# Kernel tuning notes

Measured on AMD Instinct MI355X. Metric: run time of the kernel, lower is better.

## Reference

```python
import jax, jax.numpy as jnp
import numpy as np

B, N, D, H, SEEDS = 32, 2048, 256, 8, 32
DH = D // H
SCALE = 1.0 / np.sqrt(D)  # 1/sqrt(dim_V), as in MAB


def setup_inputs() -> dict:
    key = jax.random.key(0)
    ks = jax.random.split(key, 7)
    w_std = 1.0 / np.sqrt(D)  # ~ xavier scale for (D, D)
    x = jax.random.normal(ks[0], (B, N, D), dtype=jnp.float32)
    lengths = jax.random.randint(ks[1], (B,), 1, N + 1).astype(jnp.int64)
    S = jax.random.normal(ks[2], (1, SEEDS, D), dtype=jnp.float32) * w_std
    Wq = jax.random.normal(ks[3], (D, D), dtype=jnp.float32) * w_std
    Wk = jax.random.normal(ks[4], (D, D), dtype=jnp.float32) * w_std
    Wv = jax.random.normal(ks[5], (D, D), dtype=jnp.float32) * w_std
    Wo = jax.random.normal(ks[6], (D, D), dtype=jnp.float32) * w_std
    return {"x": x, "lengths": lengths, "S": S, "Wq": Wq, "Wk": Wk, "Wv": Wv, "Wo": Wo}


def reference(x, lengths, S, Wq, Wk, Wv, Wo):
    # PMA with norm=None: seeds attend over the (length-masked) input set.
    b, n, d = x.shape
    seeds = S.shape[1]
    # Linear projections (torch Linear: y = x @ W.T, bias=False)
    Q = jnp.einsum("bsd,ed->bse", jnp.broadcast_to(S, (b, seeds, d)), Wq)  # (B,SEEDS,D)
    K = jnp.einsum("bnd,ed->bne", x, Wk)  # (B,N,D)
    V = jnp.einsum("bnd,ed->bne", x, Wv)
    # mask=['K'] -> zero K,V rows beyond lengths
    col_mask = (jnp.arange(n)[None, :] < lengths[:, None]).astype(x.dtype)  # (B,N)
    K = K * col_mask[:, :, None]
    V = V * col_mask[:, :, None]
    # head split: (h b) s d  <=>  b h s d
    Qh = Q.reshape(b, seeds, H, DH).transpose(0, 2, 1, 3)  # (B,H,SEEDS,DH)
    Kh = K.reshape(b, n, H, DH).transpose(0, 2, 1, 3)      # (B,H,N,DH)
    Vh = V.reshape(b, n, H, DH).transpose(0, 2, 1, 3)
    scores = jnp.einsum("bhsd,bhnd->bhsn", Qh, Kh) * SCALE  # (B,H,SEEDS,N)
    exp = jnp.exp(scores)
    # set_softmax: two-sided length masks, normalize over keys with +1e-15
    row_mask = (jnp.arange(seeds)[None, :] < lengths[:, None]).astype(x.dtype)  # (B,SEEDS)
    exp = exp * row_mask[:, None, :, None] * col_mask[:, None, None, :]
    A = exp / (exp.sum(axis=3, keepdims=True) + 1e-15)
    Oh = Qh + jnp.einsum("bhsn,bhnd->bhsd", A, Vh)  # residual on Q_
    O = Oh.transpose(0, 2, 1, 3).reshape(b, seeds, d)  # merge heads
    # norm0/norm1 are None (norm=None in PMA)
    O = O + jax.nn.relu(jnp.einsum("bse,de->bsd", O, Wo))
    O = O * row_mask[:, :, None]  # final apply_masks(O, lengths)
    lengths_out = jnp.minimum(jnp.full_like(lengths, seeds), lengths)
    return O, lengths_out
```

## Files before the change

### kernel.cpp

```cpp
#include <hip/hip_runtime.h>
#include <hip/hip_bf16.h>
#include <cstdint>

#define BATCH 32
#define NKEY 2048
#define DIM 256
#define NHEAD 8
#define SEEDS 32
#define DHEAD 32
#define SCALE 0.0625f
#define NCHUNK 16
#define KCH 128
#define KT 32
#define PART_BYTES 17408

typedef unsigned short u16;
typedef __attribute__((ext_vector_type(8))) short s16x8;
typedef __attribute__((ext_vector_type(8))) unsigned short u16x8;
typedef __attribute__((ext_vector_type(4))) unsigned short u16x4;
typedef __attribute__((ext_vector_type(4))) float f32x4;

__device__ __forceinline__ u16 f2bf(float f) {
    unsigned u = __float_as_uint(f);
    u += 0x7FFFu + ((u >> 16) & 1u);
    return (u16)(u >> 16);
}
__device__ __forceinline__ float bf2f(u16 h) {
    return __uint_as_float(((unsigned)h) << 16);
}
__device__ __forceinline__ int get_len(const int* lens, int b) {
    return (lens[1] == 0) ? lens[2 * b] : lens[b];
}
__device__ __forceinline__ u16x8 cvt8(const float* p) {
    f32x4 a = *(const f32x4*)p;
    f32x4 b = *(const f32x4*)(p + 4);
    u16x8 r;
    r[0] = f2bf(a[0]); r[1] = f2bf(a[1]); r[2] = f2bf(a[2]); r[3] = f2bf(a[3]);
    r[4] = f2bf(b[0]); r[5] = f2bf(b[1]); r[6] = f2bf(b[2]); r[7] = f2bf(b[3]);
    return r;
}
__device__ __forceinline__ void glds16(const u16* g, u16* l) {
    __builtin_amdgcn_global_load_lds(
        (const __attribute__((address_space(1))) unsigned int*)g,
        (__attribute__((address_space(3))) unsigned int*)l, 16, 0, 0);
}

#define XGROUPS 2097152
#define WGROUPS 16384
#define CVTBLK 2048
__global__ __launch_bounds__(256) void cvt_kernel(const float* __restrict__ x,
                                                  const float* __restrict__ Wk,
                                                  const float* __restrict__ Wv,
                                                  const float* __restrict__ S,
                                                  const float* __restrict__ Wq,
                                                  u16* __restrict__ xb,
                                                  u16* __restrict__ wb,
                                                  float* __restrict__ qf) {
    if (blockIdx.x >= CVTBLK) {
        int s = blockIdx.x - CVTBLK;
        int e = threadIdx.x;
        __shared__ float srow[DIM];
        srow[e] = S[s * DIM + e];
        __syncthreads();
        const float* wr = Wq + (size_t)e * DIM;
        float acc = 0.f;
#pragma unroll 4
        for (int d = 0; d < DIM; d += 4) {
            f32x4 w = *(const f32x4*)(wr + d);
            acc += srow[d] * w[0] + srow[d + 1] * w[1] + srow[d + 2] * w[2] + srow[d + 3] * w[3];
        }
        qf[s * DIM + e] = acc;
        return;
    }
    size_t g = (size_t)blockIdx.x * 256 + threadIdx.x;
    const size_t stride = (size_t)CVTBLK * 256;
    for (; g < XGROUPS + WGROUPS; g += stride) {
        const float* src;
        u16* dst;
        if (g < XGROUPS) {
            src = x + g * 8;
            dst = xb + g * 8;
        } else {
            size_t gw = g - XGROUPS;
            dst = wb + gw * 8;
            src = (gw < 8192) ? (Wk + gw * 8) : (Wv + (gw - 8192) * 8);
        }
        *(u16x8*)dst = cvt8(src);
    }
}

#define BM 128
#define BN 128
#define BK 32

__global__ __launch_bounds__(256) void kv_gemm_kernel(const u16* __restrict__ xb,
                                                      const u16* __restrict__ wb,
                                                      u16* __restrict__ kg,
                                                      u16* __restrict__ vt) {
    __shared__ u16 Alds[2][BM * BK];
    __shared__ u16 Blds[2][BM * BK];
    int bid = blockIdx.x;
    int swz = (bid & 7) * 256 + (bid >> 3);
    int nb = swz & 3;
    int mb = swz >> 2;
    const u16* asrc = xb + (size_t)mb * BM * DIM;
    const u16* bsrc = wb + (size_t)nb * BN * DIM;

    int tid = threadIdx.x;
    int lane = tid & 63;
    int wid = tid >> 6;
    int wr = wid >> 1, wc = wid & 1;
    int k8 = (lane >> 4) * 8;
    int fr = lane & 15;

    int srow = wid * 32 + (lane >> 2);
    int scol = (lane & 3) * 8;
    const u16* ga0 = asrc + (size_t)srow * DIM + scol;
    const u16* gb0 = bsrc + (size_t)srow * DIM + scol;

    f32x4 acc[4][4];
#pragma unroll
    for (int m = 0; m < 4; m++)
#pragma unroll
        for (int n = 0; n < 4; n++) acc[m][n] = (f32x4){0.f, 0.f, 0.f, 0.f};

    glds16(ga0,            &Alds[0][(wid * 32) * BK]);
    glds16(ga0 + 16 * DIM, &Alds[0][(wid * 32 + 16) * BK]);
    glds16(gb0,            &Blds[0][(wid * 32) * BK]);
    glds16(gb0 + 16 * DIM, &Blds[0][(wid * 32 + 16) * BK]);
    __syncthreads();

    for (int t = 0; t < DIM / BK; t++) {
        int cur = t & 1;
        if (t + 1 < DIM / BK) {
            const u16* ga = ga0 + (t + 1) * BK;
            const u16* gb = gb0 + (t + 1) * BK;
            glds16(ga,            &Alds[cur ^ 1][(wid * 32) * BK]);
            glds16(ga + 16 * DIM, &Alds[cur ^ 1][(wid * 32 + 16) * BK]);
            glds16(gb,            &Blds[cur ^ 1][(wid * 32) * BK]);
            glds16(gb + 16 * DIM, &Blds[cur ^ 1][(wid * 32 + 16) * BK]);
        }
        s16x8 af[4], bfg[4];
#pragma unroll
        for (int m = 0; m < 4; m++)
            af[m] = *(const s16x8*)&Alds[cur][(wr * 64 + m * 16 + fr) * BK + k8];
#pragma unroll
        for (int n = 0; n < 4; n++)
            bfg[n] = *(const s16x8*)&Blds[cur][(wc * 64 + n * 16 + fr) * BK + k8];
#pragma unroll
        for (int m = 0; m < 4; m++)
#pragma unroll
            for (int n = 0; n < 4; n++)
                acc[m][n] = __builtin_amdgcn_mfma_f32_16x16x32_bf16(af[m], bfg[n], acc[m][n], 0, 0, 0);
        __syncthreads();
    }

    int gmbase = mb * BM + wr * 64 + (lane >> 4) * 4;
    int gnbase = nb * BN + wc * 64 + fr;
#pragma unroll
    for (int m = 0; m < 4; m++) {
        int r0 = gmbase + m * 16;
#pragma unroll
        for (int n = 0; n < 4; n++) {
            int gc = gnbase + n * 16;
            if (gc < 256) {
#pragma unroll
                for (int q = 0; q < 4; q++) {
                    int r = r0 + q;
                    kg[(size_t)r * 256 + (gc ^ ((r & 7) << 3))] = f2bf(acc[m][n][q]);
                }
            } else {
                int dh = gc - 256;
                int bidx = r0 >> 11, key = r0 & 2047;
                u16x4 v = {f2bf(acc[m][n][0]), f2bf(acc[m][n][1]),
                           f2bf(acc[m][n][2]), f2bf(acc[m][n][3])};
                *(u16x4*)&vt[((size_t)bidx * 256 + dh) * NKEY + key] = v;
            }
        }
    }
}

__global__ __launch_bounds__(512) void attn_kernel(const u16* __restrict__ kg,
                                                   const u16* __restrict__ vt,
                                                   const float* __restrict__ qf,
                                                   const int* __restrict__ lens,
                                                   char* __restrict__ partials) {
    int b = blockIdx.y, chunk = blockIdx.x;
    int len = get_len(lens, b);
    int n0 = chunk * KCH;
    int n1 = min(n0 + KCH, len);
    int tid = threadIdx.x;
    int lane = tid & 63;
    int h = tid >> 6;
    int fr = lane & 15;
    int g = lane >> 4;
    int k8 = g * 8;

    __shared__ u16 Klds[2][KT * 256];
    __shared__ u16 VTlds[2][256 * KT];
    __shared__ u16 Plds[NHEAD][32][32];

    s16x8 qb[2];
    qb[0] = (s16x8)cvt8(qf + (size_t)(fr) * DIM + h * DHEAD + k8);
    qb[1] = (s16x8)cvt8(qf + (size_t)(16 + fr) * DIM + h * DHEAD + k8);

    f32x4 accp[2][2];
#pragma unroll
    for (int i = 0; i < 2; i++)
#pragma unroll
        for (int j = 0; j < 2; j++) accp[i][j] = (f32x4){0.f, 0.f, 0.f, 0.f};
    float dsum[2] = {0.f, 0.f};

    int nk = n1 - n0;
    int nsteps = (nk > 0) ? ((nk + KT - 1) / KT) : 0;

    const u16* gk0 = kg + ((size_t)(b * NKEY + n0 + h * 4) + (lane >> 5)) * 256 + (lane & 31) * 8;
    const u16* gv0 = vt + ((size_t)b * 256 + h * 32 + (lane >> 2)) * NKEY + n0 + (lane & 3) * 8;

    if (nsteps > 0) {
        glds16(gk0,             &Klds[0][(h * 4) * 256]);
        glds16(gk0 + 2 * 256,   &Klds[0][(h * 4 + 2) * 256]);
        glds16(gv0,             &VTlds[0][(h * 32) * KT]);
        glds16(gv0 + 16 * NKEY, &VTlds[0][(h * 32 + 16) * KT]);
        __syncthreads();
    }

    for (int t = 0; t < nsteps; t++) {
        int cur = t & 1;
        if (t + 1 < nsteps) {
            const u16* gk = gk0 + (size_t)(t + 1) * KT * 256;
            const u16* gv = gv0 + (t + 1) * KT;
            glds16(gk,             &Klds[cur ^ 1][(h * 4) * 256]);
            glds16(gk + 2 * 256,   &Klds[cur ^ 1][(h * 4 + 2) * 256]);
            glds16(gv,             &VTlds[cur ^ 1][(h * 32) * KT]);
            glds16(gv + 16 * NKEY, &VTlds[cur ^ 1][(h * 32 + 16) * KT]);
        }

        int rem = nk - t * KT;

        s16x8 ka[2];
#pragma unroll
        for (int m = 0; m < 2; m++)
            ka[m] = *(const s16x8*)&Klds[cur][(m * 16 + fr) * 256 + (((h * 4 + g) ^ (fr & 7)) << 3)];
        f32x4 sc[2][2];
#pragma unroll
        for (int m = 0; m < 2; m++)
#pragma unroll
            for (int n = 0; n < 2; n++) {
                f32x4 z = (f32x4){0.f, 0.f, 0.f, 0.f};
                sc[m][n] = __builtin_amdgcn_mfma_f32_16x16x32_bf16(ka[m], qb[n], z, 0, 0, 0);
            }

#pragma unroll
        for (int m = 0; m < 2; m++) {
            int kbase = m * 16 + g * 4;
            int col = (((kbase >> 3) ^ (fr & 3)) << 3) + (kbase & 7);
#pragma unroll
            for (int n = 0; n < 2; n++) {
                u16x4 pv;
#pragma unroll
                for (int q = 0; q < 4; q++) {
                    float e = (kbase + q < rem) ? __expf(sc[m][n][q] * SCALE) : 0.f;
                    dsum[n] += e;
                    pv[q] = f2bf(e);
                }
                *(u16x4*)&Plds[h][n * 16 + fr][col] = pv;
            }
        }

        s16x8 pa[2], vb[2];
        int rcol = (g ^ (fr & 3)) << 3;
#pragma unroll
        for (int m = 0; m < 2; m++)
            pa[m] = *(const s16x8*)&Plds[h][m * 16 + fr][rcol];
#pragma unroll
        for (int n = 0; n < 2; n++)
            vb[n] = *(const s16x8*)&VTlds[cur][(h * 32 + n * 16 + fr) * KT + k8];
#pragma unroll
        for (int m = 0; m < 2; m++)
#pragma unroll
            for (int n = 0; n < 2; n++)
                accp[m][n] = __builtin_amdgcn_mfma_f32_16x16x32_bf16(pa[m], vb[n], accp[m][n], 0, 0, 0);
        __syncthreads();
    }

    dsum[0] += __shfl_xor(dsum[0], 16);
    dsum[0] += __shfl_xor(dsum[0], 32);
    dsum[1] += __shfl_xor(dsum[1], 16);
    dsum[1] += __shfl_xor(dsum[1], 32);

    char* pb = partials + ((size_t)b * NCHUNK + chunk) * PART_BYTES;
    u16* pnum = (u16*)pb;
    float* pden = (float*)(pb + 16384);
#pragma unroll
    for (int m = 0; m < 2; m++)
#pragma unroll
        for (int n = 0; n < 2; n++)
#pragma unroll
            for (int q = 0; q < 4; q++)
                pnum[(size_t)(m * 16 + g * 4 + q) * DIM + h * DHEAD + n * 16 + fr] =
                    f2bf(accp[m][n][q]);
    if (lane < 16) {
        pden[h * 32 + fr] = dsum[0];
        pden[h * 32 + 16 + fr] = dsum[1];
    }
}

__global__ __launch_bounds__(256) void reduce_kernel(const char* __restrict__ partials,
                                                     const float* __restrict__ qf,
                                                     const int* __restrict__ lens,
                                                     float* __restrict__ opre,
                                                     float* __restrict__ outlen) {
    int b = blockIdx.x;
    int p = threadIdx.x;
    int h = p >> 5, s = p & 31;
    float denom = 0.f;
    float num[DHEAD];
#pragma unroll
    for (int j = 0; j < DHEAD; j++) num[j] = 0.f;
    for (int c = 0; c < NCHUNK; c++) {
        const char* pb = partials + ((size_t)b * NCHUNK + c) * PART_BYTES;
        denom += ((const float*)(pb + 16384))[p];
        const u16* pn = (const u16*)pb;
#pragma unroll
        for (int j = 0; j < DHEAD; j += 8) {
            u16x8 u = *(const u16x8*)&pn[(size_t)s * DIM + h * DHEAD + j];
#pragma unroll
            for (int t = 0; t < 8; t++) num[j + t] += bf2f(u[t]);
        }
    }
    float inv = 1.f / (denom + 1e-15f);
    size_t obase = ((size_t)b * SEEDS + s) * DIM + h * DHEAD;
#pragma unroll
    for (int j = 0; j < DHEAD; j++) {
        opre[obase + j] = qf[s * DIM + h * DHEAD + j] + num[j] * inv;
    }
    if (p == 0) outlen[b] = (float)min(SEEDS, get_len(lens, b));
}

__global__ __launch_bounds__(256) void epilogue_kernel(const float* __restrict__ opre,
                                                       const float* __restrict__ Wo,
                                                       const int* __restrict__ lens,
                                                       float* __restrict__ out) {
    int s = blockIdx.x, b = blockIdx.y;
    int d = threadIdx.x;
    size_t rbase = ((size_t)b * SEEDS + s) * DIM;
    if (s >= get_len(lens, b)) {
        out[rbase + d] = 0.f;
        return;
    }
    __shared__ float orow[DIM];
    orow[d] = opre[rbase + d];
    __syncthreads();
    const float* wrow = Wo + (size_t)d * DIM;
    float acc = 0.f;
#pragma unroll 4
    for (int e = 0; e < DIM; e += 4) {
        f32x4 w = *(const f32x4*)(wrow + e);
        acc += orow[e] * w[0] + orow[e + 1] * w[1] + orow[e + 2] * w[2] + orow[e + 3] * w[3];
    }
    out[rbase + d] = orow[d] + fmaxf(acc, 0.f);
}

extern "C" void kernel_launch(void* const* d_in, const int* in_sizes, int n_in,
                              void* d_out, int out_size, void* d_ws, size_t ws_size,
                              hipStream_t stream) {
    const float* x  = (const float*)d_in[0];
    const int* lens = (const int*)d_in[1];
    const float* S  = (const float*)d_in[2];
    const float* Wq = (const float*)d_in[3];
    const float* Wk = (const float*)d_in[4];
    const float* Wv = (const float*)d_in[5];
    const float* Wo = (const float*)d_in[6];
    float* out = (float*)d_out;

    char* ws = (char*)d_ws;
    float* qf       = (float*)ws;
    float* opre     = (float*)(ws + 0x8000);
    u16*   wb       = (u16*)  (ws + 0x108000);
    u16*   xb       = (u16*)  (ws + 0x148000);
    char*  partials = (char*) (ws + 0x148000);
    u16*   kg       = (u16*)  (ws + 0x2148000);
    u16*   vt       = (u16*)  (ws + 0x4148000);

    cvt_kernel<<<dim3(CVTBLK + SEEDS), 256, 0, stream>>>(x, Wk, Wv, S, Wq, xb, wb, qf);
    kv_gemm_kernel<<<dim3(2048), 256, 0, stream>>>(xb, wb, kg, vt);
    attn_kernel<<<dim3(NCHUNK, BATCH), 512, 0, stream>>>(kg, vt, qf, lens, partials);
    reduce_kernel<<<dim3(BATCH), 256, 0, stream>>>(partials, qf, lens, opre,
                                                   out + (size_t)BATCH * SEEDS * DIM);
    epilogue_kernel<<<dim3(SEEDS, BATCH), 256, 0, stream>>>(opre, Wo, lens, out);
}
```

Measured before the change: 207.3 us.

## Fuse fp32-to-bf16 conversion of x into the K/V projection GEMM A-tile load

The separate pass that converted all of x to bf16 in a workspace buffer is removed. The GEMM now loads fp32 x tiles into registers, converts them, and writes bf16 into LDS, prefetching the next step's tile during the MFMAs. This removes a full write and re-read of the 32 MB bf16 copy of x and leaves a smaller kernel that only converts the weights. In exchange, each GEMM block reads the A tile as fp32, which doubles A-side read bytes compared with bf16, and the conversion is now done for each of the 4 N-blocks. It also adds register pressure and conversion ALU work inside the main loop.

```diff
diff --git a/kernel.cpp b/kernel.cpp
--- a/kernel.cpp
+++ b/kernel.cpp
@@ -39,61 +39,50 @@
     r[4] = f2bf(b[0]); r[5] = f2bf(b[1]); r[6] = f2bf(b[2]); r[7] = f2bf(b[3]);
     return r;
 }
+__device__ __forceinline__ u16x4 cvt4(f32x4 a) {
+    u16x4 r;
+    r[0] = f2bf(a[0]); r[1] = f2bf(a[1]); r[2] = f2bf(a[2]); r[3] = f2bf(a[3]);
+    return r;
+}
 __device__ __forceinline__ void glds16(const u16* g, u16* l) {
     __builtin_amdgcn_global_load_lds(
         (const __attribute__((address_space(1))) unsigned int*)g,
         (__attribute__((address_space(3))) unsigned int*)l, 16, 0, 0);
 }
 
-#define XGROUPS 2097152
-#define WGROUPS 16384
-#define CVTBLK 2048
-__global__ __launch_bounds__(256) void cvt_kernel(const float* __restrict__ x,
-                                                  const float* __restrict__ Wk,
-                                                  const float* __restrict__ Wv,
-                                                  const float* __restrict__ S,
-                                                  const float* __restrict__ Wq,
-                                                  u16* __restrict__ xb,
-                                                  u16* __restrict__ wb,
-                                                  float* __restrict__ qf) {
-    if (blockIdx.x >= CVTBLK) {
-        int s = blockIdx.x - CVTBLK;
-        int e = threadIdx.x;
-        __shared__ float srow[DIM];
-        srow[e] = S[s * DIM + e];
-        __syncthreads();
-        const float* wr = Wq + (size_t)e * DIM;
-        float acc = 0.f;
+__global__ __launch_bounds__(256) void wcvt_kernel(const float* __restrict__ Wk,
+                                                   const float* __restrict__ Wv,
+                                                   const float* __restrict__ S,
+                                                   const float* __restrict__ Wq,
+                                                   u16* __restrict__ wb,
+                                                   float* __restrict__ qf) {
+    if (blockIdx.x < 64) {
+        size_t gw = (size_t)blockIdx.x * 256 + threadIdx.x;
+        const float* src = (gw < 8192) ? (Wk + gw * 8) : (Wv + (gw - 8192) * 8);
+        *(u16x8*)(wb + gw * 8) = cvt8(src);
+        return;
+    }
+    int s = blockIdx.x - 64;
+    int e = threadIdx.x;
+    __shared__ float srow[DIM];
+    srow[e] = S[s * DIM + e];
+    __syncthreads();
+    const float* wr = Wq + (size_t)e * DIM;
+    float acc = 0.f;
 #pragma unroll 4
-        for (int d = 0; d < DIM; d += 4) {
-            f32x4 w = *(const f32x4*)(wr + d);
-            acc += srow[d] * w[0] + srow[d + 1] * w[1] + srow[d + 2] * w[2] + srow[d + 3] * w[3];
-        }
-        qf[s * DIM + e] = acc;
-        return;
-    }
-    size_t g = (size_t)blockIdx.x * 256 + threadIdx.x;
-    const size_t stride = (size_t)CVTBLK * 256;
-    for (; g < XGROUPS + WGROUPS; g += stride) {
-        const float* src;
-        u16* dst;
-        if (g < XGROUPS) {
-            src = x + g * 8;
-            dst = xb + g * 8;
-        } else {
-            size_t gw = g - XGROUPS;
-            dst = wb + gw * 8;
-            src = (gw < 8192) ? (Wk + gw * 8) : (Wv + (gw - 8192) * 8);
-        }
-        *(u16x8*)dst = cvt8(src);
-    }
+    for (int d = 0; d < DIM; d += 4) {
+        f32x4 w = *(const f32x4*)(wr + d);
+        acc += srow[d] * w[0] + srow[d + 1] * w[1] + srow[d + 2] * w[2] + srow[d + 3] * w[3];
+    }
+    qf[s * DIM + e] = acc;
 }
 
 #define BM 128
 #define BN 128
 #define BK 32
-
-__global__ __launch_bounds__(256) void kv_gemm_kernel(const u16* __restrict__ xb,
+#define NSTEP (DIM / BK)
+
+__global__ __launch_bounds__(256) void kv_gemm_kernel(const float* __restrict__ x,
                                                       const u16* __restrict__ wb,
                                                       u16* __restrict__ kg,
                                                       u16* __restrict__ vt) {
@@ -103,7 +92,6 @@
     int swz = (bid & 7) * 256 + (bid >> 3);
     int nb = swz & 3;
     int mb = swz >> 2;
-    const u16* asrc = xb + (size_t)mb * BM * DIM;
     const u16* bsrc = wb + (size_t)nb * BN * DIM;
 
     int tid = threadIdx.x;
@@ -113,9 +101,12 @@
     int k8 = (lane >> 4) * 8;
     int fr = lane & 15;
 
+    int ar = tid >> 3;
+    int ac = (tid & 7) * 4;
+    const float* ax = x + ((size_t)mb * BM + ar) * DIM + ac;
+
     int srow = wid * 32 + (lane >> 2);
     int scol = (lane & 3) * 8;
-    const u16* ga0 = asrc + (size_t)srow * DIM + scol;
     const u16* gb0 = bsrc + (size_t)srow * DIM + scol;
 
     f32x4 acc[4][4];
@@ -124,19 +115,24 @@
 #pragma unroll
         for (int n = 0; n < 4; n++) acc[m][n] = (f32x4){0.f, 0.f, 0.f, 0.f};
 
-    glds16(ga0,            &Alds[0][(wid * 32) * BK]);
-    glds16(ga0 + 16 * DIM, &Alds[0][(wid * 32 + 16) * BK]);
+    f32x4 areg[4];
+#pragma unroll
+    for (int w = 0; w < 4; w++)
+        areg[w] = *(const f32x4*)(ax + (size_t)w * 32 * DIM);
     glds16(gb0,            &Blds[0][(wid * 32) * BK]);
     glds16(gb0 + 16 * DIM, &Blds[0][(wid * 32 + 16) * BK]);
+#pragma unroll
+    for (int w = 0; w < 4; w++)
+        *(u16x4*)&Alds[0][(w * 32 + ar) * BK + ac] = cvt4(areg[w]);
     __syncthreads();
 
-    for (int t = 0; t < DIM / BK; t++) {
+    for (int t = 0; t < NSTEP; t++) {
         int cur = t & 1;
-        if (t + 1 < DIM / BK) {
-            const u16* ga = ga0 + (t + 1) * BK;
+        if (t + 1 < NSTEP) {
+#pragma unroll
+            for (int w = 0; w < 4; w++)
+                areg[w] = *(const f32x4*)(ax + (size_t)w * 32 * DIM + (t + 1) * BK);
             const u16* gb = gb0 + (t + 1) * BK;
-            glds16(ga,            &Alds[cur ^ 1][(wid * 32) * BK]);
-            glds16(ga + 16 * DIM, &Alds[cur ^ 1][(wid * 32 + 16) * BK]);
             glds16(gb,            &Blds[cur ^ 1][(wid * 32) * BK]);
             glds16(gb + 16 * DIM, &Blds[cur ^ 1][(wid * 32 + 16) * BK]);
         }
@@ -152,6 +148,11 @@
 #pragma unroll
             for (int n = 0; n < 4; n++)
                 acc[m][n] = __builtin_amdgcn_mfma_f32_16x16x32_bf16(af[m], bfg[n], acc[m][n], 0, 0, 0);
+        if (t + 1 < NSTEP) {
+#pragma unroll
+            for (int w = 0; w < 4; w++)
+                *(u16x4*)&Alds[cur ^ 1][(w * 32 + ar) * BK + ac] = cvt4(areg[w]);
+        }
         __syncthreads();
     }
 
@@ -378,13 +379,12 @@
     float* qf       = (float*)ws;
     float* opre     = (float*)(ws + 0x8000);
     u16*   wb       = (u16*)  (ws + 0x108000);
-    u16*   xb       = (u16*)  (ws + 0x148000);
     char*  partials = (char*) (ws + 0x148000);
     u16*   kg       = (u16*)  (ws + 0x2148000);
     u16*   vt       = (u16*)  (ws + 0x4148000);
 
-    cvt_kernel<<<dim3(CVTBLK + SEEDS), 256, 0, stream>>>(x, Wk, Wv, S, Wq, xb, wb, qf);
-    kv_gemm_kernel<<<dim3(2048), 256, 0, stream>>>(xb, wb, kg, vt);
+    wcvt_kernel<<<dim3(96), 256, 0, stream>>>(Wk, Wv, S, Wq, wb, qf);
+    kv_gemm_kernel<<<dim3(2048), 256, 0, stream>>>(x, wb, kg, vt);
     attn_kernel<<<dim3(NCHUNK, BATCH), 512, 0, stream>>>(kg, vt, qf, lens, partials);
     reduce_kernel<<<dim3(BATCH), 256, 0, stream>>>(partials, qf, lens, opre,
                                                    out + (size_t)BATCH * SEEDS * DIM);
```

Result: slower. 216.6 us (+4.5%).
